# Kernel tuning notes

Hardware: AMD Instinct MI355X
Metric: run time of the kernel (lower is better)

The kernel has to match this reference:

```python
import jax, jax.numpy as jnp
import numpy as np

N_NODES = 100000
N_GRAPHS = 64


def gcn_conv(x, src, dst, W, b, num_nodes):
    """PyG GCNConv: add self-loops, symmetric deg normalization, aggregate at dst."""
    h = x @ W  # [N, out]
    ones_e = jnp.ones(src.shape[0], dtype=x.dtype)
    # degree includes self-loop (+1)
    deg = jax.ops.segment_sum(ones_e, dst, num_segments=num_nodes) + 1.0
    dinv = jnp.where(deg > 0, 1.0 / jnp.sqrt(deg), 0.0)  # deg>=1 always here
    norm = dinv[src] * dinv[dst]  # [E]
    msg = h[src] * norm[:, None]  # gather + scale
    agg = jax.ops.segment_sum(msg, dst, num_segments=num_nodes)
    # self-loop contribution: norm_ii = dinv[i]^2
    agg = agg + h * (dinv * dinv)[:, None]
    return agg + b


def global_mean_pool(x, batch, num_graphs):
    sums = jax.ops.segment_sum(x, batch, num_segments=num_graphs)
    counts = jax.ops.segment_sum(jnp.ones(x.shape[0], dtype=x.dtype), batch,
                                 num_segments=num_graphs)
    return sums / jnp.maximum(counts, 1.0)[:, None]


def setup_inputs() -> dict:
    key = jax.random.key(0)
    ks = jax.random.split(key, 8)
    H = 128
    x = jax.random.normal(ks[0], (N_NODES, 4), dtype=jnp.float32)
    edge_index = jax.random.randint(ks[1], (2, 1600000), 0, N_NODES, dtype=jnp.int64 if jax.config.read('jax_enable_x64') else jnp.int32)
    batch = jnp.sort(jax.random.randint(ks[2], (N_NODES,), 0, N_GRAPHS))
    def glorot(k, shape):
        fan_in, fan_out = shape
        lim = np.sqrt(6.0 / (fan_in + fan_out))
        return jax.random.uniform(k, shape, jnp.float32, -lim, lim)
    return {
        'x': x,
        'edge_index': edge_index,
        'batch': batch,
        'W1': glorot(ks[3], (4, H)), 'b1': jnp.zeros((H,), jnp.float32),
        'W2': glorot(ks[4], (H, H)), 'b2': jnp.zeros((H,), jnp.float32),
        'W3': glorot(ks[5], (H, H)), 'b3': jnp.zeros((H,), jnp.float32),
        'Wl': glorot(ks[6], (H, 2)), 'bl': jnp.zeros((2,), jnp.float32),
    }


def reference(x, edge_index, batch, W1, b1, W2, b2, W3, b3, Wl, bl):
    src, dst = edge_index[0], edge_index[1]
    h = jax.nn.relu(gcn_conv(x, src, dst, W1, b1, N_NODES))
    h = jax.nn.relu(gcn_conv(h, src, dst, W2, b2, N_NODES))
    h = jax.nn.relu(gcn_conv(h, src, dst, W3, b3, N_NODES))
    g = global_mean_pool(h, batch, N_GRAPHS)  # [G, H]
    logits = g @ Wl + bl  # [G, 2]
    return jax.nn.log_softmax(logits, axis=1)
```

## Files before the change

### kernel.cpp

```cpp
#include <hip/hip_runtime.h>

#define HDIM 128
#define NGRAPH 64

#define BSHIFT 9
#define NBUCK 196
#define BCAP 48
#define BSTR 49
#define RCAP 9216
#define BIN_CHUNK 4096

typedef __attribute__((ext_vector_type(8))) short short8;
typedef __attribute__((ext_vector_type(4))) float floatx4;
typedef __attribute__((ext_vector_type(2))) float floatx2;
typedef __attribute__((ext_vector_type(4))) unsigned int uintx4;

__device__ __forceinline__ float bf2f(unsigned short u) {
    union { unsigned int i; float f; } v;
    v.i = ((unsigned int)u) << 16;
    return v.f;
}
__device__ __forceinline__ unsigned short f2bf(float f) {
    unsigned int u = __float_as_uint(f);
    u += 0x7FFFu + ((u >> 16) & 1u);
    return (unsigned short)(u >> 16);
}


__global__ __launch_bounds__(256) void k_misc(int* __restrict__ gcur,
                                              const int* __restrict__ batch,
                                              float* __restrict__ gcnt,
                                              float* __restrict__ gsum,
                                              const float* __restrict__ W2,
                                              unsigned short* __restrict__ Wp2,
                                              const float* __restrict__ W3,
                                              unsigned short* __restrict__ Wp3,
                                              int N, int nbuck) {
    int t = threadIdx.x;
    int blk = blockIdx.x;
    if (blk == 0) {
        if (t < nbuck) gcur[t] = t * RCAP;
        for (int i = t; i < NGRAPH * 128; i += 256) gsum[i] = 0.f;
        if (t < NGRAPH) {
            int g = t;
            int lo = 0, hi = N;
            while (lo < hi) { int m = (lo + hi) >> 1; if (batch[m] < g) lo = m + 1; else hi = m; }
            int lb = lo;
            lo = 0; hi = N;
            while (lo < hi) { int m = (lo + hi) >> 1; if (batch[m] < g + 1) lo = m + 1; else hi = m; }
            gcnt[g] = (float)(lo - lb);
        }
        return;
    }
    const float* W = (blk <= 64) ? W2 : W3;
    unsigned short* Wp = (blk <= 64) ? Wp2 : Wp3;
    int idx = ((blk <= 64) ? (blk - 1) : (blk - 65)) * 256 + t;
    int j = idx & 7, l = (idx >> 3) & 63, frag = idx >> 9;
    int c = frag >> 2, ks = frag & 3;
    int k = ks * 32 + ((l >> 4) & 3) * 8 + j;
    int n = c * 16 + (l & 15);
    Wp[idx] = f2bf(W[k * 128 + n]);
}


__global__ __launch_bounds__(256) void k_binA(const int* __restrict__ src,
                                              const int* __restrict__ dst,
                                              int* __restrict__ gcur,
                                              unsigned int* __restrict__ binned, int E) {
    __shared__ unsigned int bin[NBUCK * BSTR];
    __shared__ int bcnt[NBUCK];
    __shared__ int bbase[NBUCK];
    int t = threadIdx.x;
    for (int b = t; b < NBUCK; b += 256) bcnt[b] = 0;
    __syncthreads();
    int e0 = blockIdx.x * BIN_CHUNK;
    #pragma unroll
    for (int i = 0; i < BIN_CHUNK / 1024; i++) {
        int e = e0 + i * 1024 + t * 4;
        if (e + 3 < E) {
            const int4 d4 = *(const int4*)&dst[e];
            const int4 s4 = *(const int4*)&src[e];
            int dd[4] = {d4.x, d4.y, d4.z, d4.w};
            int ss[4] = {s4.x, s4.y, s4.z, s4.w};
            #pragma unroll
            for (int k = 0; k < 4; k++) {
                int d = dd[k];
                unsigned int rec = ((unsigned int)(d & 511) << 20) | (unsigned int)ss[k];
                int b = d >> BSHIFT;
                int idx = atomicAdd(&bcnt[b], 1);
                if (idx < BCAP) bin[b * BSTR + idx] = rec;
                else { int p = atomicAdd(&gcur[b], 1); binned[p] = rec; }
            }
        } else {
            for (int k = 0; k < 4; k++) {
                int e2 = e + k;
                if (e2 < E) {
                    int d = dst[e2];
                    unsigned int rec = ((unsigned int)(d & 511) << 20) | (unsigned int)src[e2];
                    int b = d >> BSHIFT;
                    int idx = atomicAdd(&bcnt[b], 1);
                    if (idx < BCAP) bin[b * BSTR + idx] = rec;
                    else { int p = atomicAdd(&gcur[b], 1); binned[p] = rec; }
                }
            }
        }
    }
    __syncthreads();
    if (t < NBUCK) {
        int cnt = min(bcnt[t], BCAP);
        bbase[t] = atomicAdd(&gcur[t], cnt);
    }
    __syncthreads();
    int wave = t >> 6, lane = t & 63;
    for (int b = wave; b < NBUCK; b += 4) {
        int cnt = min(bcnt[b], BCAP);
        int base = bbase[b];
        if (lane < cnt) binned[base + lane] = bin[b * BSTR + lane];
    }
}

__global__ __launch_bounds__(256) void k_fillB(const int* __restrict__ gcur,
                                               const unsigned int* __restrict__ binned,
                                               int* __restrict__ P,
                                               float* __restrict__ dinv,
                                               int* __restrict__ csr,
                                               const float4* __restrict__ x4,
                                               float4* __restrict__ xs4,
                                               int N, int nbuck) {
    __shared__ int ps[256];
    __shared__ int cnt[512];
    __shared__ int image[RCAP];
    int b = blockIdx.x;
    int t = threadIdx.x;
    int lt = (t < nbuck) ? (gcur[t] - t * RCAP) : 0;
    ps[t] = lt;
    __syncthreads();
    for (int d = 1; d < 256; d <<= 1) {
        int o = (t >= d) ? ps[t - d] : 0;
        __syncthreads();
        ps[t] += o;
        __syncthreads();
    }
    int start = (b > 0) ? ps[b - 1] : 0;
    int len = ps[b] - start;
    __syncthreads();

    int n0 = b << BSHIFT;
    int nloc = min(n0 + 512, N) - n0;
    cnt[t] = 0; cnt[t + 256] = 0;
    __syncthreads();
    const unsigned int* rb = binned + (size_t)b * RCAP;
    for (int i = t; i < len; i += 256) atomicAdd(&cnt[rb[i] >> 20], 1);
    __syncthreads();
    int c0 = cnt[2 * t], c1 = cnt[2 * t + 1];
    int pair = c0 + c1;
    __syncthreads();
    cnt[t] = pair;
    __syncthreads();
    for (int d = 1; d < 256; d <<= 1) {
        int o = (t >= d) ? cnt[t - d] : 0;
        __syncthreads();
        cnt[t] += o;
        __syncthreads();
    }
    int excl = cnt[t] - pair;
    __syncthreads();
    if (2 * t < nloc) {
        int n = n0 + 2 * t;
        float dv0 = rsqrtf((float)c0 + 1.0f);
        P[n] = start + excl;
        dinv[n] = dv0;
        float4 xv = x4[n];
        xs4[n] = make_float4(xv.x * dv0, xv.y * dv0, xv.z * dv0, xv.w * dv0);
    }
    if (2 * t + 1 < nloc) {
        int n = n0 + 2 * t + 1;
        float dv1 = rsqrtf((float)c1 + 1.0f);
        P[n] = start + excl + c0;
        dinv[n] = dv1;
        float4 xv = x4[n];
        xs4[n] = make_float4(xv.x * dv1, xv.y * dv1, xv.z * dv1, xv.w * dv1);
    }
    if (b == nbuck - 1 && t == 0) P[N] = start + len;
    cnt[2 * t] = excl;
    cnt[2 * t + 1] = excl + c0;
    __syncthreads();
    for (int i = t; i < len; i += 256) {
        unsigned int rec = rb[i];
        int pos = atomicAdd(&cnt[rec >> 20], 1);
        image[pos] = (int)(rec & 0xFFFFFu);
    }
    __syncthreads();
    for (int i = t; i < len; i += 256) csr[start + i] = image[i];
}

__global__ void k_aggx_csr(const int* __restrict__ P, const int* __restrict__ csr,
                           const float4* __restrict__ xs, const float* __restrict__ dinv,
                           float4* __restrict__ aggx, int N) {
    int d = blockIdx.x * blockDim.x + threadIdx.x;
    if (d >= N) return;
    int s0 = P[d], s1 = P[d + 1];
    float dd = dinv[d];
    float4 sv = xs[d];
    float4 a = make_float4(sv.x * dd, sv.y * dd, sv.z * dd, sv.w * dd);
    int i = s0;
    int pre = min(s1, (s0 + 3) & ~3);
    for (; i < pre; i++) {
        float4 v = xs[csr[i]];
        a.x += v.x; a.y += v.y; a.z += v.z; a.w += v.w;
    }
    for (; i + 8 <= s1; i += 8) {
        const int4 iA = *(const int4*)&csr[i];
        const int4 iB = *(const int4*)&csr[i + 4];
        float4 vA = xs[iA.x], vB = xs[iA.y], vC = xs[iA.z], vD = xs[iA.w];
        float4 vE = xs[iB.x], vF = xs[iB.y], vG = xs[iB.z], vH = xs[iB.w];
        a.x += vA.x + vB.x + vC.x + vD.x + vE.x + vF.x + vG.x + vH.x;
        a.y += vA.y + vB.y + vC.y + vD.y + vE.y + vF.y + vG.y + vH.y;
        a.z += vA.z + vB.z + vC.z + vD.z + vE.z + vF.z + vG.z + vH.z;
        a.w += vA.w + vB.w + vC.w + vD.w + vE.w + vF.w + vG.w + vH.w;
    }
    for (; i + 4 <= s1; i += 4) {
        const int4 ix = *(const int4*)&csr[i];
        float4 vA = xs[ix.x], vB = xs[ix.y], vC = xs[ix.z], vD = xs[ix.w];
        a.x += vA.x + vB.x + vC.x + vD.x;
        a.y += vA.y + vB.y + vC.y + vD.y;
        a.z += vA.z + vB.z + vC.z + vD.z;
        a.w += vA.w + vB.w + vC.w + vD.w;
    }
    for (; i < s1; i++) {
        float4 v = xs[csr[i]];
        a.x += v.x; a.y += v.y; a.z += v.z; a.w += v.w;
    }
    aggx[d] = make_float4(a.x * dd, a.y * dd, a.z * dd, a.w * dd);
}

#define LXS 136
__global__ __launch_bounds__(256) void k_l1t2(const float4* __restrict__ aggx,
                                              const float* __restrict__ W1,
                                              const float* __restrict__ b1,
                                              const unsigned short* __restrict__ Wp,
                                              const float* __restrict__ dinv,
                                              unsigned char* __restrict__ out8, int N) {
    __shared__ unsigned short lx[64 * LXS];
    __shared__ unsigned short lw[16384];
    __shared__ float w1s[512];
    __shared__ float b1s[128];
    __shared__ float ax[64][4];
    int t = threadIdx.x;
    int n0 = blockIdx.x * 64;

    for (int i = t; i < 512; i += 256) w1s[i] = W1[i];
    if (t < 128) b1s[t] = b1[t];
    if (t < 64) {
        float4 v = (n0 + t < N) ? aggx[n0 + t] : make_float4(0.f, 0.f, 0.f, 0.f);
        ax[t][0] = v.x; ax[t][1] = v.y; ax[t][2] = v.z; ax[t][3] = v.w;
    }
    for (int ch = t; ch < 2048; ch += 256)
        *(uint4*)&lw[ch * 8] = *(const uint4*)&Wp[ch * 8];
    __syncthreads();

    for (int i = t; i < 8192; i += 256) {
        int n = i >> 7, j = i & 127;
        float v = b1s[j] + ax[n][0] * w1s[j] + ax[n][1] * w1s[128 + j]
                         + ax[n][2] * w1s[256 + j] + ax[n][3] * w1s[384 + j];
        lx[n * LXS + j] = f2bf(fmaxf(v, 0.f));
    }
    __syncthreads();

    int w = t >> 6, lane = t & 63;
    int m0 = w * 16;
    int col = lane & 15, quad = lane >> 4;

    short8 afrag[4];
    #pragma unroll
    for (int ks = 0; ks < 4; ks++)
        afrag[ks] = *(const short8*)&lx[(m0 + col) * LXS + ks * 32 + quad * 8];

    float dv[4];
    #pragma unroll
    for (int r = 0; r < 4; r++) {
        int gn = n0 + m0 + quad * 4 + r;
        dv[r] = (gn < N) ? dinv[gn] : 0.0f;
    }

    #pragma unroll
    for (int c = 0; c < 8; c++) {
        floatx4 acc = {0.f, 0.f, 0.f, 0.f};
        #pragma unroll
        for (int ks = 0; ks < 4; ks++) {
            const short8 bfrag = *(const short8*)&lw[((c * 4 + ks) * 64 + lane) * 8];
            acc = __builtin_amdgcn_mfma_f32_16x16x32_bf16(afrag[ks], bfrag, acc, 0, 0, 0);
        }
        int j = c * 16 + col;
        size_t sbase = (size_t)(j >> 5) * N * 32 + (size_t)(j & 31);
        #pragma unroll
        for (int r = 0; r < 4; r++) {
            int gn = n0 + m0 + quad * 4 + r;
            if (gn < N) {
                float v = acc[r] * dv[r];
                out8[sbase + (size_t)gn * 32] =
                    (unsigned char)(__builtin_amdgcn_cvt_pk_fp8_f32(v, v, 0, false) & 0xFF);
            }
        }
    }
}

__global__ __launch_bounds__(256) void k_transform_mfma(const unsigned short* __restrict__ in,
                                                        const unsigned short* __restrict__ Wp,
                                                        const float* __restrict__ dinv,
                                                        unsigned char* __restrict__ out8, int N) {
    __shared__ unsigned short lx[64 * LXS];
    __shared__ unsigned short lw[16384];
    int t = threadIdx.x;
    int n0 = blockIdx.x * 64;

    for (int ch = t; ch < 1024; ch += 256) {
        int row = ch >> 4, part = ch & 15;
        uint4 val = make_uint4(0, 0, 0, 0);
        if (n0 + row < N) val = *(const uint4*)&in[(size_t)(n0 + row) * 128 + part * 8];
        *(uint4*)&lx[row * LXS + part * 8] = val;
    }
    for (int ch = t; ch < 2048; ch += 256)
        *(uint4*)&lw[ch * 8] = *(const uint4*)&Wp[ch * 8];
    __syncthreads();

    int w = t >> 6, lane = t & 63;
    int m0 = w * 16;
    int col = lane & 15, quad = lane >> 4;

    short8 afrag[4];
    #pragma unroll
    for (int ks = 0; ks < 4; ks++)
        afrag[ks] = *(const short8*)&lx[(m0 + col) * LXS + ks * 32 + quad * 8];

    float dv[4];
    #pragma unroll
    for (int r = 0; r < 4; r++) {
        int gn = n0 + m0 + quad * 4 + r;
        dv[r] = (gn < N) ? dinv[gn] : 0.0f;
    }

    #pragma unroll
    for (int c = 0; c < 8; c++) {
        floatx4 acc = {0.f, 0.f, 0.f, 0.f};
        #pragma unroll
        for (int ks = 0; ks < 4; ks++) {
            const short8 bfrag = *(const short8*)&lw[((c * 4 + ks) * 64 + lane) * 8];
            acc = __builtin_amdgcn_mfma_f32_16x16x32_bf16(afrag[ks], bfrag, acc, 0, 0, 0);
        }
        int j = c * 16 + col;
        size_t sbase = (size_t)(j >> 5) * N * 32 + (size_t)(j & 31);
        #pragma unroll
        for (int r = 0; r < 4; r++) {
            int gn = n0 + m0 + quad * 4 + r;
            if (gn < N) {
                float v = acc[r] * dv[r];
                out8[sbase + (size_t)gn * 32] =
                    (unsigned char)(__builtin_amdgcn_cvt_pk_fp8_f32(v, v, 0, false) & 0xFF);
            }
        }
    }
}

__device__ __forceinline__ void dec16(uint4 u, float* a) {
    floatx2 p;
    p = __builtin_amdgcn_cvt_pk_f32_fp8(u.x, false); a[0] += p.x; a[1] += p.y;
    p = __builtin_amdgcn_cvt_pk_f32_fp8(u.x, true);  a[2] += p.x; a[3] += p.y;
    p = __builtin_amdgcn_cvt_pk_f32_fp8(u.y, false); a[4] += p.x; a[5] += p.y;
    p = __builtin_amdgcn_cvt_pk_f32_fp8(u.y, true);  a[6] += p.x; a[7] += p.y;
    p = __builtin_amdgcn_cvt_pk_f32_fp8(u.z, false); a[8] += p.x; a[9] += p.y;
    p = __builtin_amdgcn_cvt_pk_f32_fp8(u.z, true);  a[10] += p.x; a[11] += p.y;
    p = __builtin_amdgcn_cvt_pk_f32_fp8(u.w, false); a[12] += p.x; a[13] += p.y;
    p = __builtin_amdgcn_cvt_pk_f32_fp8(u.w, true);  a[14] += p.x; a[15] += p.y;
}

__global__ __launch_bounds__(256) void k_agg_sl(const int* __restrict__ P,
                                                const int* __restrict__ csr,
                                                const unsigned int* __restrict__ tab,
                                                const float* __restrict__ dinv,
                                                const float* __restrict__ bias,
                                                unsigned short* __restrict__ out16,
                                                const int* __restrict__ batch,
                                                float* __restrict__ gsum,
                                                int N, int mode) {
    __shared__ float psum[32][32];
    int t = threadIdx.x;
    int bid = blockIdx.x;
    int xcd = bid & 7;
    int slice = xcd >> 1;
    int chunk = (bid >> 3) * 2 + (xcd & 1);
    int nb = chunk * 32;
    int grp = t >> 3;
    int lg = t & 7;
    int slot = lg >> 1;
    int half = lg & 1;
    int g = nb + grp;
    const unsigned int* sl = tab + (size_t)slice * N * 8;
    int hofs = half * 4;

    float a[16];
    #pragma unroll
    for (int j = 0; j < 16; j++) a[j] = 0.f;

    if (g < N) {
        int s0 = P[g], s1 = P[g + 1];
        int i = s0;
        int a0 = min(s1, (s0 + 3) & ~3);
        if (i < a0) {
            int k = i + slot;
            if (k < a0) {
                int e = csr[k];
                uint4 u = *(const uint4*)&sl[(size_t)e * 8 + hofs];
                dec16(u, a);
            }
            i = a0;
        }
        for (; i + 8 <= s1; i += 8) {
            const int4 iv0 = *(const int4*)&csr[i];
            const int4 iv1 = *(const int4*)&csr[i + 4];
            int e0 = (slot & 1) ? ((slot & 2) ? iv0.w : iv0.y)
                                : ((slot & 2) ? iv0.z : iv0.x);
            int e1 = (slot & 1) ? ((slot & 2) ? iv1.w : iv1.y)
                                : ((slot & 2) ? iv1.z : iv1.x);
            uint4 u0 = *(const uint4*)&sl[(size_t)e0 * 8 + hofs];
            uint4 u1 = *(const uint4*)&sl[(size_t)e1 * 8 + hofs];
            dec16(u0, a);
            dec16(u1, a);
        }
        for (; i + 4 <= s1; i += 4) {
            const int4 iv = *(const int4*)&csr[i];
            int e = (slot & 1) ? ((slot & 2) ? iv.w : iv.y)
                               : ((slot & 2) ? iv.z : iv.x);
            uint4 u = *(const uint4*)&sl[(size_t)e * 8 + hofs];
            dec16(u, a);
        }
        if (i < s1) {
            int k = i + slot;
            if (k < s1) {
                int e = csr[k];
                uint4 u = *(const uint4*)&sl[(size_t)e * 8 + hofs];
                dec16(u, a);
            }
        }
        if (slot == 0) {
            uint4 su = *(const uint4*)&sl[(size_t)g * 8 + hofs];
            dec16(su, a);
        }
    }

    #pragma unroll
    for (int j = 0; j < 16; j++) {
        a[j] += __shfl_xor(a[j], 2);
        a[j] += __shfl_xor(a[j], 4);
    }

    float o[16];
    #pragma unroll
    for (int j = 0; j < 16; j++) o[j] = 0.f;
    if (g < N) {
        float dd = dinv[g];
        const float* bb = &bias[slice * 32 + half * 16];
        #pragma unroll
        for (int j = 0; j < 16; j++) o[j] = fmaxf(a[j] * dd + bb[j], 0.f);
        if (mode == 0 && slot == 0) {
            uintx4 w0, w1;
            w0.x = (unsigned int)f2bf(o[0]) | ((unsigned int)f2bf(o[1]) << 16);
            w0.y = (unsigned int)f2bf(o[2]) | ((unsigned int)f2bf(o[3]) << 16);
            w0.z = (unsigned int)f2bf(o[4]) | ((unsigned int)f2bf(o[5]) << 16);
            w0.w = (unsigned int)f2bf(o[6]) | ((unsigned int)f2bf(o[7]) << 16);
            w1.x = (unsigned int)f2bf(o[8]) | ((unsigned int)f2bf(o[9]) << 16);
            w1.y = (unsigned int)f2bf(o[10]) | ((unsigned int)f2bf(o[11]) << 16);
            w1.z = (unsigned int)f2bf(o[12]) | ((unsigned int)f2bf(o[13]) << 16);
            w1.w = (unsigned int)f2bf(o[14]) | ((unsigned int)f2bf(o[15]) << 16);
            unsigned short* dst = &out16[(size_t)g * 128 + slice * 32 + half * 16];
            __builtin_nontemporal_store(w0, (uintx4*)dst);
            __builtin_nontemporal_store(w1, (uintx4*)(dst + 8));
        }
    }
    if (mode != 0) {
        if (slot == 0) {
            #pragma unroll
            for (int q = 0; q < 4; q++)
                *(float4*)&psum[grp][half * 16 + q * 4] =
                    make_float4(o[q * 4], o[q * 4 + 1], o[q * 4 + 2], o[q * 4 + 3]);
        }
        __syncthreads();
        if (t < 32 && nb < N) {
            int f = t;
            int nbN = min(32, N - nb);
            int b0 = batch[nb], bL = batch[nb + nbN - 1];
            if (b0 == bL) {
                float s = 0.f;
                #pragma unroll
                for (int n = 0; n < 32; n++) s += psum[n][f];
                unsafeAtomicAdd(&gsum[(size_t)b0 * 128 + slice * 32 + f], s);
            } else {
                float acc = 0.f; int cur = b0;
                for (int n = 0; n < nbN; n++) {
                    int bb = batch[nb + n];
                    if (bb != cur) {
                        unsafeAtomicAdd(&gsum[(size_t)cur * 128 + slice * 32 + f], acc);
                        acc = 0.f; cur = bb;
                    }
                    acc += psum[n][f];
                }
                unsafeAtomicAdd(&gsum[(size_t)cur * 128 + slice * 32 + f], acc);
            }
        }
    }
}

__global__ __launch_bounds__(256) void k_head(const float* __restrict__ gsum,
                                              const float* __restrict__ gcnt,
                                              const float* __restrict__ Wl,
                                              const float* __restrict__ bl,
                                              float* __restrict__ out, int G) {
    int t = threadIdx.x;
    int g = t >> 2, q = t & 3;
    if (g >= G) return;
    float l0 = 0.f, l1 = 0.f;
    #pragma unroll
    for (int k = 0; k < 32; k++) {
        int jj = q * 32 + k;
        float v = gsum[(size_t)g * 128 + jj];
        l0 += v * Wl[jj * 2 + 0];
        l1 += v * Wl[jj * 2 + 1];
    }
    l0 += __shfl_xor(l0, 1, 64); l1 += __shfl_xor(l1, 1, 64);
    l0 += __shfl_xor(l0, 2, 64); l1 += __shfl_xor(l1, 2, 64);
    if (q == 0) {
        float inv = 1.0f / fmaxf(gcnt[g], 1.0f);
        l0 = l0 * inv + bl[0];
        l1 = l1 * inv + bl[1];
        float m = fmaxf(l0, l1);
        float lse = m + logf(expf(l0 - m) + expf(l1 - m));
        out[g * 2 + 0] = l0 - lse;
        out[g * 2 + 1] = l1 - lse;
    }
}


extern "C" void kernel_launch(void* const* d_in, const int* in_sizes, int n_in,
                              void* d_out, int out_size, void* d_ws, size_t ws_size,
                              hipStream_t stream) {
    const float* x   = (const float*)d_in[0];
    const int*   ei  = (const int*)d_in[1];
    const int*   bat = (const int*)d_in[2];
    const float* W1  = (const float*)d_in[3];
    const float* b1  = (const float*)d_in[4];
    const float* W2  = (const float*)d_in[5];
    const float* b2  = (const float*)d_in[6];
    const float* W3  = (const float*)d_in[7];
    const float* b3  = (const float*)d_in[8];
    const float* Wl  = (const float*)d_in[9];
    const float* bl  = (const float*)d_in[10];

    const int N = in_sizes[0] / 4;
    const int E = in_sizes[1] / 2;
    const int* srcI = ei;
    const int* dstI = ei + E;

    const int nbuck = (N + 511) >> BSHIFT;
    const int pAlloc = ((N + 1 + 3) & ~3) + 4;

    float* wsf  = (float*)d_ws;
    float* dinv = wsf;
    int*   P    = (int*)(dinv + N);
    int*   csr  = P + pAlloc;
    float* aggx = (float*)(csr + E);
    unsigned short* bufA16 = (unsigned short*)(aggx + (size_t)N * 4);
    unsigned char*  hs8    = (unsigned char*)(bufA16 + (size_t)N * 128);
    unsigned short* Wp2    = (unsigned short*)(hs8 + (size_t)N * 128);
    unsigned short* Wp3    = Wp2 + 16384;
    float* gsum = (float*)(Wp3 + 16384);
    float* gcnt = gsum + NGRAPH * 128;
    int*   gcur = (int*)(gcnt + NGRAPH);
    unsigned int* binned = (unsigned int*)hs8;
    float* xs4 = (float*)bufA16;

    const int chunks = (N + 31) >> 5;
    const int aggGrid = ((chunks + 1) >> 1) * 8;

    k_misc<<<129, 256, 0, stream>>>(gcur, bat, gcnt, gsum, W2, Wp2, W3, Wp3, N, nbuck);
    k_binA<<<(E + BIN_CHUNK - 1) / BIN_CHUNK, 256, 0, stream>>>(srcI, dstI, gcur, binned, E);
    k_fillB<<<nbuck, 256, 0, stream>>>(gcur, binned, P, dinv, csr,
                                       (const float4*)x, (float4*)xs4, N, nbuck);

    k_aggx_csr<<<(N + 255) / 256, 256, 0, stream>>>(P, csr, (const float4*)xs4, dinv,
                                                    (float4*)aggx, N);
    k_l1t2<<<(N + 63) / 64, 256, 0, stream>>>((const float4*)aggx, W1, b1, Wp2, dinv, hs8, N);

    k_agg_sl<<<aggGrid, 256, 0, stream>>>(P, csr, (const unsigned int*)hs8,
                                          dinv, b2, bufA16, nullptr, nullptr, N, 0);

    k_transform_mfma<<<(N + 63) / 64, 256, 0, stream>>>(bufA16, Wp3, dinv, hs8, N);
    k_agg_sl<<<aggGrid, 256, 0, stream>>>(P, csr, (const unsigned int*)hs8,
                                          dinv, b3, nullptr, bat, gsum, N, 1);

    k_head<<<1, 256, 0, stream>>>(gsum, gcnt, Wl, bl, (float*)d_out, NGRAPH);
}
```

Measured before the change: 315.8 us.

## Split layer-1 CSR aggregation across four lanes per node and pack fp8 accumulators

The first-layer 4-wide aggregation now assigns four threads per destination node instead of one. Each lane strides over that node's edges, and the partial sums are combined with xor shuffles. This targets load imbalance and the long serial gather chains per thread, at the cost of four times as many threads and some shuffle overhead. The fp8 aggregation kernel also drops its alignment prologue and int4 index selects in favour of per-slot scalar index loads. It accumulates into packed float2 vectors, which enables packed adds, and shuffles them as 64-bit values to halve the shuffle count.

```diff
diff --git a/kernel.cpp b/kernel.cpp
--- a/kernel.cpp
+++ b/kernel.cpp
@@ -194,44 +194,35 @@
     for (int i = t; i < len; i += 256) csr[start + i] = image[i];
 }
 
-__global__ void k_aggx_csr(const int* __restrict__ P, const int* __restrict__ csr,
-                           const float4* __restrict__ xs, const float* __restrict__ dinv,
-                           float4* __restrict__ aggx, int N) {
-    int d = blockIdx.x * blockDim.x + threadIdx.x;
+__global__ void k_aggx4(const int* __restrict__ P, const int* __restrict__ csr,
+                        const float4* __restrict__ xs, const float* __restrict__ dinv,
+                        float4* __restrict__ aggx, int N) {
+    int idx = blockIdx.x * blockDim.x + threadIdx.x;
+    int d = idx >> 2, l = idx & 3;
     if (d >= N) return;
     int s0 = P[d], s1 = P[d + 1];
-    float dd = dinv[d];
-    float4 sv = xs[d];
-    float4 a = make_float4(sv.x * dd, sv.y * dd, sv.z * dd, sv.w * dd);
-    int i = s0;
-    int pre = min(s1, (s0 + 3) & ~3);
-    for (; i < pre; i++) {
+    float ax = 0.f, ay = 0.f, az = 0.f, aw = 0.f;
+    int i = s0 + l;
+    for (; i + 4 < s1; i += 8) {
+        int e0 = csr[i], e1 = csr[i + 4];
+        float4 v0 = xs[e0], v1 = xs[e1];
+        ax += v0.x + v1.x; ay += v0.y + v1.y;
+        az += v0.z + v1.z; aw += v0.w + v1.w;
+    }
+    if (i < s1) {
         float4 v = xs[csr[i]];
-        a.x += v.x; a.y += v.y; a.z += v.z; a.w += v.w;
-    }
-    for (; i + 8 <= s1; i += 8) {
-        const int4 iA = *(const int4*)&csr[i];
-        const int4 iB = *(const int4*)&csr[i + 4];
-        float4 vA = xs[iA.x], vB = xs[iA.y], vC = xs[iA.z], vD = xs[iA.w];
-        float4 vE = xs[iB.x], vF = xs[iB.y], vG = xs[iB.z], vH = xs[iB.w];
-        a.x += vA.x + vB.x + vC.x + vD.x + vE.x + vF.x + vG.x + vH.x;
-        a.y += vA.y + vB.y + vC.y + vD.y + vE.y + vF.y + vG.y + vH.y;
-        a.z += vA.z + vB.z + vC.z + vD.z + vE.z + vF.z + vG.z + vH.z;
-        a.w += vA.w + vB.w + vC.w + vD.w + vE.w + vF.w + vG.w + vH.w;
-    }
-    for (; i + 4 <= s1; i += 4) {
-        const int4 ix = *(const int4*)&csr[i];
-        float4 vA = xs[ix.x], vB = xs[ix.y], vC = xs[ix.z], vD = xs[ix.w];
-        a.x += vA.x + vB.x + vC.x + vD.x;
-        a.y += vA.y + vB.y + vC.y + vD.y;
-        a.z += vA.z + vB.z + vC.z + vD.z;
-        a.w += vA.w + vB.w + vC.w + vD.w;
-    }
-    for (; i < s1; i++) {
-        float4 v = xs[csr[i]];
-        a.x += v.x; a.y += v.y; a.z += v.z; a.w += v.w;
-    }
-    aggx[d] = make_float4(a.x * dd, a.y * dd, a.z * dd, a.w * dd);
+        ax += v.x; ay += v.y; az += v.z; aw += v.w;
+    }
+    ax += __shfl_xor(ax, 1); ay += __shfl_xor(ay, 1);
+    az += __shfl_xor(az, 1); aw += __shfl_xor(aw, 1);
+    ax += __shfl_xor(ax, 2); ay += __shfl_xor(ay, 2);
+    az += __shfl_xor(az, 2); aw += __shfl_xor(aw, 2);
+    if (l == 0) {
+        float dd = dinv[d];
+        float4 sv = xs[d];
+        aggx[d] = make_float4((ax + sv.x * dd) * dd, (ay + sv.y * dd) * dd,
+                              (az + sv.z * dd) * dd, (aw + sv.w * dd) * dd);
+    }
 }
 
 #define LXS 136
@@ -362,16 +353,15 @@
     }
 }
 
-__device__ __forceinline__ void dec16(uint4 u, float* a) {
-    floatx2 p;
-    p = __builtin_amdgcn_cvt_pk_f32_fp8(u.x, false); a[0] += p.x; a[1] += p.y;
-    p = __builtin_amdgcn_cvt_pk_f32_fp8(u.x, true);  a[2] += p.x; a[3] += p.y;
-    p = __builtin_amdgcn_cvt_pk_f32_fp8(u.y, false); a[4] += p.x; a[5] += p.y;
-    p = __builtin_amdgcn_cvt_pk_f32_fp8(u.y, true);  a[6] += p.x; a[7] += p.y;
-    p = __builtin_amdgcn_cvt_pk_f32_fp8(u.z, false); a[8] += p.x; a[9] += p.y;
-    p = __builtin_amdgcn_cvt_pk_f32_fp8(u.z, true);  a[10] += p.x; a[11] += p.y;
-    p = __builtin_amdgcn_cvt_pk_f32_fp8(u.w, false); a[12] += p.x; a[13] += p.y;
-    p = __builtin_amdgcn_cvt_pk_f32_fp8(u.w, true);  a[14] += p.x; a[15] += p.y;
+__device__ __forceinline__ void dec8x2(uint4 u, floatx2* a) {
+    a[0] += __builtin_amdgcn_cvt_pk_f32_fp8(u.x, false);
+    a[1] += __builtin_amdgcn_cvt_pk_f32_fp8(u.x, true);
+    a[2] += __builtin_amdgcn_cvt_pk_f32_fp8(u.y, false);
+    a[3] += __builtin_amdgcn_cvt_pk_f32_fp8(u.y, true);
+    a[4] += __builtin_amdgcn_cvt_pk_f32_fp8(u.z, false);
+    a[5] += __builtin_amdgcn_cvt_pk_f32_fp8(u.z, true);
+    a[6] += __builtin_amdgcn_cvt_pk_f32_fp8(u.w, false);
+    a[7] += __builtin_amdgcn_cvt_pk_f32_fp8(u.w, true);
 }
 
 __global__ __launch_bounds__(256) void k_agg_sl(const int* __restrict__ P,
@@ -398,60 +388,48 @@
     const unsigned int* sl = tab + (size_t)slice * N * 8;
     int hofs = half * 4;
 
-    float a[16];
-    #pragma unroll
-    for (int j = 0; j < 16; j++) a[j] = 0.f;
+    floatx2 a2[8];
+    #pragma unroll
+    for (int j = 0; j < 8; j++) a2[j] = (floatx2){0.f, 0.f};
 
     if (g < N) {
         int s0 = P[g], s1 = P[g + 1];
         int i = s0;
-        int a0 = min(s1, (s0 + 3) & ~3);
-        if (i < a0) {
-            int k = i + slot;
-            if (k < a0) {
-                int e = csr[k];
-                uint4 u = *(const uint4*)&sl[(size_t)e * 8 + hofs];
-                dec16(u, a);
-            }
-            i = a0;
-        }
         for (; i + 8 <= s1; i += 8) {
-            const int4 iv0 = *(const int4*)&csr[i];
-            const int4 iv1 = *(const int4*)&csr[i + 4];
-            int e0 = (slot & 1) ? ((slot & 2) ? iv0.w : iv0.y)
-                                : ((slot & 2) ? iv0.z : iv0.x);
-            int e1 = (slot & 1) ? ((slot & 2) ? iv1.w : iv1.y)
-                                : ((slot & 2) ? iv1.z : iv1.x);
+            int e0 = csr[i + slot];
+            int e1 = csr[i + slot + 4];
             uint4 u0 = *(const uint4*)&sl[(size_t)e0 * 8 + hofs];
             uint4 u1 = *(const uint4*)&sl[(size_t)e1 * 8 + hofs];
-            dec16(u0, a);
-            dec16(u1, a);
-        }
-        for (; i + 4 <= s1; i += 4) {
-            const int4 iv = *(const int4*)&csr[i];
-            int e = (slot & 1) ? ((slot & 2) ? iv.w : iv.y)
-                               : ((slot & 2) ? iv.z : iv.x);
+            dec8x2(u0, a2);
+            dec8x2(u1, a2);
+        }
+        if (i + 4 <= s1) {
+            int e = csr[i + slot];
             uint4 u = *(const uint4*)&sl[(size_t)e * 8 + hofs];
-            dec16(u, a);
-        }
-        if (i < s1) {
-            int k = i + slot;
-            if (k < s1) {
-                int e = csr[k];
-                uint4 u = *(const uint4*)&sl[(size_t)e * 8 + hofs];
-                dec16(u, a);
-            }
+            dec8x2(u, a2);
+            i += 4;
+        }
+        int k = i + slot;
+        if (k < s1) {
+            int e = csr[k];
+            uint4 u = *(const uint4*)&sl[(size_t)e * 8 + hofs];
+            dec8x2(u, a2);
         }
         if (slot == 0) {
             uint4 su = *(const uint4*)&sl[(size_t)g * 8 + hofs];
-            dec16(su, a);
-        }
-    }
-
-    #pragma unroll
-    for (int j = 0; j < 16; j++) {
-        a[j] += __shfl_xor(a[j], 2);
-        a[j] += __shfl_xor(a[j], 4);
+            dec8x2(su, a2);
+        }
+    }
+
+    #pragma unroll
+    for (int j = 0; j < 8; j++) {
+        union { double d; floatx2 f; } u, v;
+        u.f = a2[j];
+        v.d = __shfl_xor(u.d, 2);
+        a2[j] += v.f;
+        u.f = a2[j];
+        v.d = __shfl_xor(u.d, 4);
+        a2[j] += v.f;
     }
 
     float o[16];
@@ -461,7 +439,10 @@
         float dd = dinv[g];
         const float* bb = &bias[slice * 32 + half * 16];
         #pragma unroll
-        for (int j = 0; j < 16; j++) o[j] = fmaxf(a[j] * dd + bb[j], 0.f);
+        for (int j = 0; j < 16; j++) {
+            float av = a2[j >> 1][j & 1];
+            o[j] = fmaxf(av * dd + bb[j], 0.f);
+        }
         if (mode == 0 && slot == 0) {
             uintx4 w0, w1;
             w0.x = (unsigned int)f2bf(o[0]) | ((unsigned int)f2bf(o[1]) << 16);
@@ -586,8 +567,8 @@
     k_fillB<<<nbuck, 256, 0, stream>>>(gcur, binned, P, dinv, csr,
                                        (const float4*)x, (float4*)xs4, N, nbuck);
 
-    k_aggx_csr<<<(N + 255) / 256, 256, 0, stream>>>(P, csr, (const float4*)xs4, dinv,
-                                                    (float4*)aggx, N);
+    k_aggx4<<<(N * 4 + 255) / 256, 256, 0, stream>>>(P, csr, (const float4*)xs4, dinv,
+                                                     (float4*)aggx, N);
     k_l1t2<<<(N + 63) / 64, 256, 0, stream>>>((const float4*)aggx, W1, b1, Wp2, dinv, hs8, N);
 
     k_agg_sl<<<aggGrid, 256, 0, stream>>>(P, csr, (const unsigned int*)hs8,
```

Result: faster. 293.2 us (-7.2%).
